# Performance work log

Hardware: AMD Instinct MI355X
Metric: run time of the kernel (lower is better)

The kernel has to match this reference:

```python
import jax, jax.numpy as jnp
import numpy as np

B, NC, CN, K, DN = 2, 256, 256, 16, 64
G, HM, HS, HMOD, MOD_OUT = 8, 128, 128, 64, 5


def setup_inputs() -> dict:
    rng = np.random.default_rng(0)
    # per-neuron top-K neighbors within cell, excluding self, sorted (matches torch buffer build)
    scores = rng.random((NC, CN, CN)).astype(np.float32)
    ii = np.arange(CN)
    scores[:, ii, ii] = -np.inf
    conn = np.argpartition(-scores, K, axis=-1)[..., :K]
    conn = np.sort(conn, axis=-1).astype(np.int32)  # [NC, CN, K]

    key = jax.random.key(0)
    ks = jax.random.split(key, 12)
    n = lambda k, s, sc=1.0: jax.random.normal(k, s, jnp.float32) * sc
    return {
        'h': n(ks[0], (B, NC, CN, DN), 0.01),
        'w_conn': n(ks[1], (B, NC, CN, K), 0.1),
        'cell_context': n(ks[2], (B, NC, DN), 0.1),
        'neuron_id': n(ks[3], (NC, CN, DN), 0.02),
        'msg_w1': n(ks[4], (G, HM, 3 * DN), 0.05), 'msg_b1': jnp.zeros((G, HM)),
        'msg_w2': n(ks[5], (G, DN, HM), 0.005), 'msg_b2': jnp.zeros((G, DN)),
        'state_w1': n(ks[6], (G, HS, 3 * DN), 0.05), 'state_b1': jnp.zeros((G, HS)),
        'state_w2': n(ks[7], (G, DN, HS), 0.005), 'state_b2': jnp.zeros((G, DN)),
        'mod_w1': n(ks[8], (NC, 2 * DN, HMOD), 0.05), 'mod_b1': jnp.zeros((NC, HMOD)),
        'mod_w2': n(ks[9], (NC, HMOD, MOD_OUT), 0.0005), 'mod_b2': jnp.zeros((NC, MOD_OUT)),
        'conn_idx': jnp.asarray(conn),
        'cell_to_group': (jnp.arange(NC) % G).astype(jnp.int32),
    }


def reference(h, w_conn, cell_context, neuron_id,
              msg_w1, msg_b1, msg_w2, msg_b2,
              state_w1, state_b1, state_w2, state_b2,
              mod_w1, mod_b1, mod_w2, mod_b2,
              conn_idx, cell_to_group):
    nc = h.shape[1]
    cell_ix = jnp.arange(nc)[:, None, None]
    # gather K-neighbor states per neuron: [B, NC, CN, K, DN]
    nb = jax.vmap(lambda hb: hb[cell_ix, conn_idx])(h)
    # connection-weighted aggregation
    agg = jnp.einsum('bnck,bnckd->bncd', w_conn, nb)

    g = cell_to_group  # [NC]
    # grouped message MLP (2-layer), per-cell weights gathered from group table
    mfeat = jnp.concatenate([h, agg, jnp.broadcast_to(neuron_id[None], h.shape)], axis=-1)
    mh = jax.nn.gelu(jnp.einsum('bncf,nhf->bnch', mfeat, msg_w1[g]) + msg_b1[g][None, :, None, :])
    msg = jnp.einsum('bnch,ndh->bncd', mh, msg_w2[g]) + msg_b2[g][None, :, None, :]

    # grouped state MLP, residual update on h
    ctx = jnp.broadcast_to(cell_context[:, :, None, :], h.shape)
    sfeat = jnp.concatenate([h, msg, ctx], axis=-1)
    sh = jax.nn.gelu(jnp.einsum('bncf,nhf->bnch', sfeat, state_w1[g]) + state_b1[g][None, :, None, :])
    h_new = h + jnp.einsum('bnch,ndh->bncd', sh, state_w2[g]) + state_b2[g][None, :, None, :]

    # per-cell modulation MLP on pooled stats (h_mean || msg_mean)
    pooled = jnp.concatenate([h_new.mean(axis=2), msg.mean(axis=2)], axis=-1)  # [B, NC, 2DN]
    ph = jax.nn.gelu(jnp.einsum('bnf,nfh->bnh', pooled, mod_w1) + mod_b1[None])
    mod = jnp.einsum('bnh,nho->bno', ph, mod_w2) + mod_b2[None]
    return h_new, msg, mod
```

## Files before the change

### kernel.cpp

```cpp
#include <hip/hip_runtime.h>

#define NC_  256
#define CN_  256
#define K_   16
#define DN_  64
#define G_   8
#define HM_  128
#define F3_  192

typedef unsigned short u16;
typedef short v8s __attribute__((ext_vector_type(8)));
typedef float v4f __attribute__((ext_vector_type(4)));


__device__ __forceinline__ u16 f2b(float f) {
    unsigned v; __builtin_memcpy(&v, &f, 4);
    v = v + 0x7fffu + ((v >> 16) & 1u);
    return (u16)(v >> 16);
}
__device__ __forceinline__ v8s cvt8(const float* p) {
    float4 a = *(const float4*)p, b = *(const float4*)(p + 4);
    v8s r;
    r[0] = (short)f2b(a.x); r[1] = (short)f2b(a.y); r[2] = (short)f2b(a.z); r[3] = (short)f2b(a.w);
    r[4] = (short)f2b(b.x); r[5] = (short)f2b(b.y); r[6] = (short)f2b(b.z); r[7] = (short)f2b(b.w);
    return r;
}
__device__ __forceinline__ float gelu_t(float x) {
    float u = x * x;
    float t = 1.5957691216057308f * x * __builtin_fmaf(0.044715f, u, 1.0f);
    float e = __expf(-t);
    return x * __builtin_amdgcn_rcpf(1.0f + e);
}

__global__ __launch_bounds__(256) void cvt_w(
    const float* __restrict__ mw1, const float* __restrict__ mw2,
    const float* __restrict__ sw1, const float* __restrict__ sw2,
    u16* __restrict__ dst)
{
    int e = (blockIdx.x * 256 + threadIdx.x) * 4;
    const float* s; int off;
    if      (e < 196608) { s = mw1; off = e; }
    else if (e < 262144) { s = mw2; off = e - 196608; }
    else if (e < 458752) { s = sw1; off = e - 262144; }
    else                 { s = sw2; off = e - 458752; }
    float4 v = *(const float4*)(s + off);
    ushort4 o4;
    o4.x = f2b(v.x); o4.y = f2b(v.y); o4.z = f2b(v.z); o4.w = f2b(v.w);
    *(ushort4*)(dst + e) = o4;
}

__global__ __launch_bounds__(256) void gth(
    const float* __restrict__ h, const float* __restrict__ wconn,
    const int* __restrict__ conn, float* __restrict__ outf)
{
    __shared__ u16 hl[16384];
    const int p    = blockIdx.x;
    const int bnc  = (p & 7) * 64 + ((p >> 3) & 63);
    const int half = p >> 9;
    const int tid  = threadIdx.x;
    const int wave = tid >> 6, lane = tid & 63;
    const int r0   = half * 128 + wave * 32;
    const int n    = bnc & 255;
    const size_t hb = (size_t)bnc * 16384;

#pragma unroll
    for (int i = 0; i < 16; ++i) {
        float4 v = *(const float4*)(h + hb + tid * 4 + i * 1024);
        ushort4 o;
        o.x = f2b(v.x); o.y = f2b(v.y); o.z = f2b(v.z); o.w = f2b(v.w);
        *(ushort4*)(hl + tid * 4 + i * 1024) = o;
    }
    __syncthreads();

    float* aggo = outf + (size_t)8388608 + hb;
    const int*   __restrict__ cp = conn  + n * 4096 + r0 * 16;
    const float* __restrict__ wp = wconn + (size_t)bnc * 4096 + (size_t)r0 * 16;
    int iv = cp[lane]; float wv = wp[lane];
    for (int g4 = 0; g4 < 8; ++g4) {
        int ivn = 0; float wvn = 0.0f;
        if (g4 < 7) { ivn = cp[(g4 + 1) * 64 + lane]; wvn = wp[(g4 + 1) * 64 + lane]; }
#pragma unroll
        for (int r = 0; r < 4; ++r) {
            float a0 = 0.0f, a1 = 0.0f;
#pragma unroll
            for (int k = 0; k < 16; k += 2) {
                const int l0 = r * 16 + k;
                int   i0 = __builtin_amdgcn_readlane(iv, l0);
                int   i1 = __builtin_amdgcn_readlane(iv, l0 + 1);
                float w0 = __int_as_float(__builtin_amdgcn_readlane(__float_as_int(wv), l0));
                float w1 = __int_as_float(__builtin_amdgcn_readlane(__float_as_int(wv), l0 + 1));
                unsigned h0 = (unsigned)hl[i0 * 64 + lane] << 16;
                unsigned h1 = (unsigned)hl[i1 * 64 + lane] << 16;
                a0 = __builtin_fmaf(w0, __uint_as_float(h0), a0);
                a1 = __builtin_fmaf(w1, __uint_as_float(h1), a1);
            }
            aggo[(size_t)(r0 + g4 * 4 + r) * 64 + lane] = a0 + a1;
        }
        iv = ivn; wv = wvn;
    }
}

__global__ __launch_bounds__(64, 4) void mg_main(
    const float* __restrict__ h,    const float* __restrict__ ctx,
    const float* __restrict__ nid,
    const u16* __restrict__ mw1b,   const float* __restrict__ mb1,
    const u16* __restrict__ mw2b,   const float* __restrict__ mb2,
    const u16* __restrict__ sw1b,   const float* __restrict__ sb1,
    const u16* __restrict__ sw2b,   const float* __restrict__ sb2,
    const int* __restrict__ c2g,
    float* __restrict__ outf,       float* __restrict__ partial)
{
    const int p     = blockIdx.x;
    const int bnc   = (p & 7) * 64 + (p >> 6);
    const int chunk = (p >> 3) & 7;
    const int r0    = chunk * 32;
    const int n     = bnc & 255;
    const int g     = c2g[n];
    const int lane  = threadIdx.x;
    const int q     = lane >> 4, ln = lane & 15;

    __shared__ u16 buf[32 * 138];

    const size_t hbase = (size_t)bnc * 16384;
    const size_t nbase = (size_t)n   * 16384;
    float* oH = outf + hbase;
    float* oM = outf + (size_t)8388608 + hbase;
    const size_t pbase = (size_t)(bnc * 8 + chunk) * 128;

    v8s hfr[2][2], gfr[2][2], nfr[2][2];
#pragma unroll
    for (int mi = 0; mi < 2; ++mi) {
        int c = r0 + mi * 16 + ln;
        hfr[mi][0] = cvt8(h   + hbase + (size_t)c * 64 +  0 + q * 8);
        hfr[mi][1] = cvt8(h   + hbase + (size_t)c * 64 + 32 + q * 8);
        gfr[mi][0] = cvt8(oM  + (size_t)c * 64 +  0 + q * 8);
        gfr[mi][1] = cvt8(oM  + (size_t)c * 64 + 32 + q * 8);
        nfr[mi][0] = cvt8(nid + nbase + (size_t)c * 64 +  0 + q * 8);
        nfr[mi][1] = cvt8(nid + nbase + (size_t)c * 64 + 32 + q * 8);
    }

    {
        v8s afr0[6] = {hfr[0][0], hfr[0][1], gfr[0][0], gfr[0][1], nfr[0][0], nfr[0][1]};
        v8s afr1[6] = {hfr[1][0], hfr[1][1], gfr[1][0], gfr[1][1], nfr[1][0], nfr[1][1]};
        float b1v[8];
#pragma unroll
        for (int nt = 0; nt < 8; ++nt) b1v[nt] = mb1[g * HM_ + nt * 16 + ln];
        const u16* w1g = mw1b + (size_t)g * HM_ * F3_;
#pragma unroll
        for (int nt = 0; nt < 8; ++nt) {
            v4f acc0 = {0,0,0,0}, acc1 = {0,0,0,0};
#pragma unroll
            for (int ks = 0; ks < 6; ++ks) {
                v8s bf = *(const v8s*)(w1g + (nt * 16 + ln) * F3_ + ks * 32 + q * 8);
                acc0 = __builtin_amdgcn_mfma_f32_16x16x32_bf16(afr0[ks], bf, acc0, 0, 0, 0);
                acc1 = __builtin_amdgcn_mfma_f32_16x16x32_bf16(afr1[ks], bf, acc1, 0, 0, 0);
            }
            int c0 = q * 4, c1 = 16 + q * 4;
#pragma unroll
            for (int r = 0; r < 4; ++r) {
                buf[(c0 + r) * 138 + nt * 16 + ln] = f2b(gelu_t(acc0[r] + b1v[nt]));
                buf[(c1 + r) * 138 + nt * 16 + ln] = f2b(gelu_t(acc1[r] + b1v[nt]));
            }
        }
    }

    {
        v8s afr[2][4];
#pragma unroll
        for (int mi = 0; mi < 2; ++mi) {
            int c = mi * 16 + ln;
#pragma unroll
            for (int ks = 0; ks < 4; ++ks)
                afr[mi][ks] = *(const v8s*)(buf + c * 138 + ks * 32 + q * 8);
        }
        const u16* w2g = mw2b + (size_t)g * DN_ * HM_;
        float mpart[4];
#pragma unroll
        for (int nt = 0; nt < 4; ++nt) {
            float bb = mb2[g * DN_ + nt * 16 + ln];
            v4f acc[2] = {{0,0,0,0},{0,0,0,0}};
#pragma unroll
            for (int ks = 0; ks < 4; ++ks) {
                v8s bf = *(const v8s*)(w2g + (nt * 16 + ln) * HM_ + ks * 32 + q * 8);
#pragma unroll
                for (int mi = 0; mi < 2; ++mi)
                    acc[mi] = __builtin_amdgcn_mfma_f32_16x16x32_bf16(afr[mi][ks], bf, acc[mi], 0, 0, 0);
            }
            float ms = 0.0f;
            int d = nt * 16 + ln;
#pragma unroll
            for (int mi = 0; mi < 2; ++mi) {
                int c = mi * 16 + q * 4;
#pragma unroll
                for (int r = 0; r < 4; ++r) {
                    float mv = acc[mi][r] + bb;
                    buf[(c + r) * 138 + d] = f2b(mv);
                    oM[(size_t)(r0 + c + r) * 64 + d] = mv;
                    ms += mv;
                }
            }
            mpart[nt] = ms;
        }
#pragma unroll
        for (int nt = 0; nt < 4; ++nt) {
            float v = mpart[nt];
            v += __shfl_xor(v, 16);
            v += __shfl_xor(v, 32);
            if (q == 0) partial[pbase + 64 + nt * 16 + ln] = v * (1.0f / 256.0f);
        }
    }

    {
        v8s cfr0 = cvt8(ctx + (size_t)bnc * DN_ +  0 + q * 8);
        v8s cfr1 = cvt8(ctx + (size_t)bnc * DN_ + 32 + q * 8);
        v8s afr[2][4];
#pragma unroll
        for (int mi = 0; mi < 2; ++mi) {
            int c = mi * 16 + ln;
            afr[mi][0] = hfr[mi][0];
            afr[mi][1] = hfr[mi][1];
            afr[mi][2] = *(const v8s*)(buf + c * 138 +  0 + q * 8);
            afr[mi][3] = *(const v8s*)(buf + c * 138 + 32 + q * 8);
        }
        float b1v[8];
#pragma unroll
        for (int nt = 0; nt < 8; ++nt) b1v[nt] = sb1[g * HM_ + nt * 16 + ln];
        const u16* w1g = sw1b + (size_t)g * HM_ * F3_;
#pragma unroll
        for (int nt = 0; nt < 8; ++nt) {
            v4f acc[2] = {{0,0,0,0},{0,0,0,0}};
#pragma unroll
            for (int ks = 0; ks < 4; ++ks) {
                v8s bf = *(const v8s*)(w1g + (nt * 16 + ln) * F3_ + ks * 32 + q * 8);
#pragma unroll
                for (int mi = 0; mi < 2; ++mi)
                    acc[mi] = __builtin_amdgcn_mfma_f32_16x16x32_bf16(afr[mi][ks], bf, acc[mi], 0, 0, 0);
            }
#pragma unroll
            for (int ks = 4; ks < 6; ++ks) {
                v8s bf = *(const v8s*)(w1g + (nt * 16 + ln) * F3_ + ks * 32 + q * 8);
                v8s aa = (ks == 4) ? cfr0 : cfr1;
#pragma unroll
                for (int mi = 0; mi < 2; ++mi)
                    acc[mi] = __builtin_amdgcn_mfma_f32_16x16x32_bf16(aa, bf, acc[mi], 0, 0, 0);
            }
#pragma unroll
            for (int mi = 0; mi < 2; ++mi) {
                int c = mi * 16 + q * 4;
#pragma unroll
                for (int r = 0; r < 4; ++r)
                    buf[(c + r) * 138 + nt * 16 + ln] = f2b(gelu_t(acc[mi][r] + b1v[nt]));
            }
        }
    }

    {
        v8s afr[2][4];
#pragma unroll
        for (int mi = 0; mi < 2; ++mi) {
            int c = mi * 16 + ln;
#pragma unroll
            for (int ks = 0; ks < 4; ++ks)
                afr[mi][ks] = *(const v8s*)(buf + c * 138 + ks * 32 + q * 8);
        }
        const u16* w2g = sw2b + (size_t)g * DN_ * HM_;
        float hpart[4];
#pragma unroll
        for (int nt = 0; nt < 4; ++nt) {
            float bb = sb2[g * DN_ + nt * 16 + ln];
            v4f acc[2] = {{0,0,0,0},{0,0,0,0}};
#pragma unroll
            for (int ks = 0; ks < 4; ++ks) {
                v8s bf = *(const v8s*)(w2g + (nt * 16 + ln) * HM_ + ks * 32 + q * 8);
#pragma unroll
                for (int mi = 0; mi < 2; ++mi)
                    acc[mi] = __builtin_amdgcn_mfma_f32_16x16x32_bf16(afr[mi][ks], bf, acc[mi], 0, 0, 0);
            }
            float hs = 0.0f;
            int d = nt * 16 + ln;
#pragma unroll
            for (int mi = 0; mi < 2; ++mi) {
                int c = mi * 16 + q * 4;
#pragma unroll
                for (int r = 0; r < 4; ++r) {
                    float hv = h[hbase + (size_t)(r0 + c + r) * 64 + d];
                    float hn = hv + acc[mi][r] + bb;
                    oH[(size_t)(r0 + c + r) * 64 + d] = hn;
                    hs += hn;
                }
            }
            hpart[nt] = hs;
        }
#pragma unroll
        for (int nt = 0; nt < 4; ++nt) {
            float v = hpart[nt];
            v += __shfl_xor(v, 16);
            v += __shfl_xor(v, 32);
            if (q == 0) partial[pbase + nt * 16 + ln] = v * (1.0f / 256.0f);
        }
    }
}

__global__ __launch_bounds__(256) void mg_mod(
    const float* __restrict__ w1, const float* __restrict__ b1,
    const float* __restrict__ w2, const float* __restrict__ b2,
    const float* __restrict__ partial, float* __restrict__ outf)
{
    __shared__ float pool[128];
    __shared__ float ph4[4][64];
    const int bnc = blockIdx.x, n = bnc & 255, t = threadIdx.x;
    if (t < 128) {
        const float* pp = partial + (size_t)bnc * 1024 + t;
        float s = 0.0f;
#pragma unroll
        for (int j = 0; j < 8; ++j) s += pp[j * 128];
        pool[t] = s;
    }
    __syncthreads();
    {
        const int col = t & 63, fh = t >> 6;
        const float* w1p = w1 + ((size_t)n * 128 + fh * 32) * 64 + col;
        float acc = 0.0f;
#pragma unroll
        for (int i = 0; i < 32; ++i)
            acc = __builtin_fmaf(pool[fh * 32 + i], w1p[(size_t)i * 64], acc);
        ph4[fh][col] = acc;
    }
    __syncthreads();
    if (t < 64) {
        float a  = ph4[0][t] + ph4[1][t] + ph4[2][t] + ph4[3][t] + b1[n * 64 + t];
        float ph = gelu_t(a);
        float part5[5];
#pragma unroll
        for (int o = 0; o < 5; ++o) part5[o] = ph * w2[((size_t)n * 64 + t) * 5 + o];
#pragma unroll
        for (int off = 32; off > 0; off >>= 1)
#pragma unroll
            for (int o = 0; o < 5; ++o) part5[o] += __shfl_down(part5[o], off);
        if (t == 0) {
#pragma unroll
            for (int o = 0; o < 5; ++o)
                outf[(size_t)16777216 + bnc * 5 + o] = part5[o] + b2[n * 5 + o];
        }
    }
}

extern "C" void kernel_launch(void* const* d_in, const int* in_sizes, int n_in,
                              void* d_out, int out_size, void* d_ws, size_t ws_size,
                              hipStream_t stream) {
    const float* h     = (const float*)d_in[0];
    const float* wconn = (const float*)d_in[1];
    const float* ctx   = (const float*)d_in[2];
    const float* nid   = (const float*)d_in[3];
    const float* mw1   = (const float*)d_in[4];
    const float* mb1   = (const float*)d_in[5];
    const float* mw2   = (const float*)d_in[6];
    const float* mb2   = (const float*)d_in[7];
    const float* sw1   = (const float*)d_in[8];
    const float* sb1   = (const float*)d_in[9];
    const float* sw2   = (const float*)d_in[10];
    const float* sb2   = (const float*)d_in[11];
    const float* dw1   = (const float*)d_in[12];
    const float* db1   = (const float*)d_in[13];
    const float* dw2   = (const float*)d_in[14];
    const float* db2   = (const float*)d_in[15];
    const int* conn    = (const int*)d_in[16];
    const int* c2g     = (const int*)d_in[17];
    float* outf    = (float*)d_out;
    u16*   wb      = (u16*)d_ws;
    float* partial = (float*)((char*)d_ws + 1048576);

    cvt_w<<<512, 256, 0, stream>>>(mw1, mw2, sw1, sw2, wb);
    gth<<<1024, 256, 0, stream>>>(h, wconn, conn, outf);
    mg_main<<<4096, 64, 0, stream>>>(h, ctx, nid,
                                     wb,           mb1,
                                     wb + 196608,  mb2,
                                     wb + 262144,  sb1,
                                     wb + 458752,  sb2,
                                     c2g, outf, partial);
    mg_mod<<<512, 256, 0, stream>>>(dw1, db1, dw2, db2, partial, outf);
}
```

Measured before the change: 243.2 us.

## Fuse neighbor gather into main MLP kernel with 64-row tiles per block

Removes the separate gather kernel. The weighted neighbor aggregation is now computed inside mg_main directly from global h, and written as bf16 into shared memory instead of round-tripping fp32 agg through the output buffer. Each 64-thread block now handles 64 rows instead of 32, with 4 MFMA row tiles, which halves the grid and the partial-sum count used by the modulation kernel. The trade-offs are per-lane scattered global loads for the gather instead of LDS reads, more registers per wave (launch bounds lowered to 2), and fewer blocks available to hide latency.

```diff
diff --git a/kernel.cpp b/kernel.cpp
--- a/kernel.cpp
+++ b/kernel.cpp
@@ -49,125 +49,104 @@
     *(ushort4*)(dst + e) = o4;
 }
 
-__global__ __launch_bounds__(256) void gth(
-    const float* __restrict__ h, const float* __restrict__ wconn,
-    const int* __restrict__ conn, float* __restrict__ outf)
-{
-    __shared__ u16 hl[16384];
-    const int p    = blockIdx.x;
-    const int bnc  = (p & 7) * 64 + ((p >> 3) & 63);
-    const int half = p >> 9;
-    const int tid  = threadIdx.x;
-    const int wave = tid >> 6, lane = tid & 63;
-    const int r0   = half * 128 + wave * 32;
-    const int n    = bnc & 255;
-    const size_t hb = (size_t)bnc * 16384;
-
-#pragma unroll
-    for (int i = 0; i < 16; ++i) {
-        float4 v = *(const float4*)(h + hb + tid * 4 + i * 1024);
-        ushort4 o;
-        o.x = f2b(v.x); o.y = f2b(v.y); o.z = f2b(v.z); o.w = f2b(v.w);
-        *(ushort4*)(hl + tid * 4 + i * 1024) = o;
-    }
-    __syncthreads();
-
-    float* aggo = outf + (size_t)8388608 + hb;
-    const int*   __restrict__ cp = conn  + n * 4096 + r0 * 16;
-    const float* __restrict__ wp = wconn + (size_t)bnc * 4096 + (size_t)r0 * 16;
-    int iv = cp[lane]; float wv = wp[lane];
-    for (int g4 = 0; g4 < 8; ++g4) {
-        int ivn = 0; float wvn = 0.0f;
-        if (g4 < 7) { ivn = cp[(g4 + 1) * 64 + lane]; wvn = wp[(g4 + 1) * 64 + lane]; }
-#pragma unroll
-        for (int r = 0; r < 4; ++r) {
-            float a0 = 0.0f, a1 = 0.0f;
-#pragma unroll
-            for (int k = 0; k < 16; k += 2) {
-                const int l0 = r * 16 + k;
-                int   i0 = __builtin_amdgcn_readlane(iv, l0);
-                int   i1 = __builtin_amdgcn_readlane(iv, l0 + 1);
-                float w0 = __int_as_float(__builtin_amdgcn_readlane(__float_as_int(wv), l0));
-                float w1 = __int_as_float(__builtin_amdgcn_readlane(__float_as_int(wv), l0 + 1));
-                unsigned h0 = (unsigned)hl[i0 * 64 + lane] << 16;
-                unsigned h1 = (unsigned)hl[i1 * 64 + lane] << 16;
-                a0 = __builtin_fmaf(w0, __uint_as_float(h0), a0);
-                a1 = __builtin_fmaf(w1, __uint_as_float(h1), a1);
-            }
-            aggo[(size_t)(r0 + g4 * 4 + r) * 64 + lane] = a0 + a1;
-        }
-        iv = ivn; wv = wvn;
-    }
-}
-
-__global__ __launch_bounds__(64, 4) void mg_main(
-    const float* __restrict__ h,    const float* __restrict__ ctx,
-    const float* __restrict__ nid,
+__global__ __launch_bounds__(64, 2) void mg_main(
+    const float* __restrict__ h,    const float* __restrict__ wconn,
+    const float* __restrict__ ctx,  const float* __restrict__ nid,
     const u16* __restrict__ mw1b,   const float* __restrict__ mb1,
     const u16* __restrict__ mw2b,   const float* __restrict__ mb2,
     const u16* __restrict__ sw1b,   const float* __restrict__ sb1,
     const u16* __restrict__ sw2b,   const float* __restrict__ sb2,
-    const int* __restrict__ c2g,
+    const int* __restrict__ conn,   const int* __restrict__ c2g,
     float* __restrict__ outf,       float* __restrict__ partial)
 {
     const int p     = blockIdx.x;
-    const int bnc   = (p & 7) * 64 + (p >> 6);
-    const int chunk = (p >> 3) & 7;
-    const int r0    = chunk * 32;
+    const int bnc   = (p & 7) * 64 + (p >> 5);
+    const int quart = (p >> 3) & 3;
+    const int r0    = quart * 64;
     const int n     = bnc & 255;
     const int g     = c2g[n];
     const int lane  = threadIdx.x;
     const int q     = lane >> 4, ln = lane & 15;
 
-    __shared__ u16 buf[32 * 138];
+    __shared__ u16 buf[64 * 138];
 
     const size_t hbase = (size_t)bnc * 16384;
     const size_t nbase = (size_t)n   * 16384;
     float* oH = outf + hbase;
     float* oM = outf + (size_t)8388608 + hbase;
-    const size_t pbase = (size_t)(bnc * 8 + chunk) * 128;
-
-    v8s hfr[2][2], gfr[2][2], nfr[2][2];
-#pragma unroll
-    for (int mi = 0; mi < 2; ++mi) {
-        int c = r0 + mi * 16 + ln;
-        hfr[mi][0] = cvt8(h   + hbase + (size_t)c * 64 +  0 + q * 8);
-        hfr[mi][1] = cvt8(h   + hbase + (size_t)c * 64 + 32 + q * 8);
-        gfr[mi][0] = cvt8(oM  + (size_t)c * 64 +  0 + q * 8);
-        gfr[mi][1] = cvt8(oM  + (size_t)c * 64 + 32 + q * 8);
+    const size_t pbase = (size_t)(bnc * 4 + quart) * 128;
+
+    {
+        const float* __restrict__ hp = h + hbase;
+        const int*   __restrict__ cp = conn  + n * 4096 + r0 * 16;
+        const float* __restrict__ wp = wconn + (size_t)bnc * 4096 + (size_t)r0 * 16;
+        int iv = cp[lane]; float wv = wp[lane];
+        for (int g4 = 0; g4 < 16; ++g4) {
+            int ivn = 0; float wvn = 0.0f;
+            if (g4 < 15) { ivn = cp[(g4 + 1) * 64 + lane]; wvn = wp[(g4 + 1) * 64 + lane]; }
+#pragma unroll
+            for (int r = 0; r < 4; ++r) {
+                float a0 = 0.0f, a1 = 0.0f;
+#pragma unroll
+                for (int k = 0; k < 16; k += 2) {
+                    const int l0 = r * 16 + k;
+                    int   i0 = __builtin_amdgcn_readlane(iv, l0);
+                    int   i1 = __builtin_amdgcn_readlane(iv, l0 + 1);
+                    float w0 = __int_as_float(__builtin_amdgcn_readlane(__float_as_int(wv), l0));
+                    float w1 = __int_as_float(__builtin_amdgcn_readlane(__float_as_int(wv), l0 + 1));
+                    a0 = __builtin_fmaf(w0, hp[i0 * 64 + lane], a0);
+                    a1 = __builtin_fmaf(w1, hp[i1 * 64 + lane], a1);
+                }
+                buf[(g4 * 4 + r) * 138 + lane] = f2b(a0 + a1);
+            }
+            iv = ivn; wv = wvn;
+        }
+    }
+
+    v8s hfr[4][2], gfr[4][2], nfr[4][2];
+#pragma unroll
+    for (int mi = 0; mi < 4; ++mi) {
+        int c  = r0 + mi * 16 + ln;
+        int lc = mi * 16 + ln;
+        hfr[mi][0] = cvt8(h + hbase + (size_t)c * 64 +  0 + q * 8);
+        hfr[mi][1] = cvt8(h + hbase + (size_t)c * 64 + 32 + q * 8);
+        gfr[mi][0] = *(const v8s*)(buf + lc * 138 +  0 + q * 8);
+        gfr[mi][1] = *(const v8s*)(buf + lc * 138 + 32 + q * 8);
         nfr[mi][0] = cvt8(nid + nbase + (size_t)c * 64 +  0 + q * 8);
         nfr[mi][1] = cvt8(nid + nbase + (size_t)c * 64 + 32 + q * 8);
     }
 
     {
-        v8s afr0[6] = {hfr[0][0], hfr[0][1], gfr[0][0], gfr[0][1], nfr[0][0], nfr[0][1]};
-        v8s afr1[6] = {hfr[1][0], hfr[1][1], gfr[1][0], gfr[1][1], nfr[1][0], nfr[1][1]};
         float b1v[8];
 #pragma unroll
         for (int nt = 0; nt < 8; ++nt) b1v[nt] = mb1[g * HM_ + nt * 16 + ln];
         const u16* w1g = mw1b + (size_t)g * HM_ * F3_;
 #pragma unroll
         for (int nt = 0; nt < 8; ++nt) {
-            v4f acc0 = {0,0,0,0}, acc1 = {0,0,0,0};
+            v4f acc[4] = {{0,0,0,0},{0,0,0,0},{0,0,0,0},{0,0,0,0}};
 #pragma unroll
             for (int ks = 0; ks < 6; ++ks) {
                 v8s bf = *(const v8s*)(w1g + (nt * 16 + ln) * F3_ + ks * 32 + q * 8);
-                acc0 = __builtin_amdgcn_mfma_f32_16x16x32_bf16(afr0[ks], bf, acc0, 0, 0, 0);
-                acc1 = __builtin_amdgcn_mfma_f32_16x16x32_bf16(afr1[ks], bf, acc1, 0, 0, 0);
-            }
-            int c0 = q * 4, c1 = 16 + q * 4;
-#pragma unroll
-            for (int r = 0; r < 4; ++r) {
-                buf[(c0 + r) * 138 + nt * 16 + ln] = f2b(gelu_t(acc0[r] + b1v[nt]));
-                buf[(c1 + r) * 138 + nt * 16 + ln] = f2b(gelu_t(acc1[r] + b1v[nt]));
-            }
-        }
-    }
-
-    {
-        v8s afr[2][4];
-#pragma unroll
-        for (int mi = 0; mi < 2; ++mi) {
+#pragma unroll
+                for (int mi = 0; mi < 4; ++mi) {
+                    v8s aa = (ks < 2) ? hfr[mi][ks] : (ks < 4) ? gfr[mi][ks - 2] : nfr[mi][ks - 4];
+                    acc[mi] = __builtin_amdgcn_mfma_f32_16x16x32_bf16(aa, bf, acc[mi], 0, 0, 0);
+                }
+            }
+#pragma unroll
+            for (int mi = 0; mi < 4; ++mi) {
+                int c = mi * 16 + q * 4;
+#pragma unroll
+                for (int r = 0; r < 4; ++r)
+                    buf[(c + r) * 138 + nt * 16 + ln] = f2b(gelu_t(acc[mi][r] + b1v[nt]));
+            }
+        }
+    }
+
+    {
+        v8s afr[4][4];
+#pragma unroll
+        for (int mi = 0; mi < 4; ++mi) {
             int c = mi * 16 + ln;
 #pragma unroll
             for (int ks = 0; ks < 4; ++ks)
@@ -178,18 +157,18 @@
 #pragma unroll
         for (int nt = 0; nt < 4; ++nt) {
             float bb = mb2[g * DN_ + nt * 16 + ln];
-            v4f acc[2] = {{0,0,0,0},{0,0,0,0}};
+            v4f acc[4] = {{0,0,0,0},{0,0,0,0},{0,0,0,0},{0,0,0,0}};
 #pragma unroll
             for (int ks = 0; ks < 4; ++ks) {
                 v8s bf = *(const v8s*)(w2g + (nt * 16 + ln) * HM_ + ks * 32 + q * 8);
 #pragma unroll
-                for (int mi = 0; mi < 2; ++mi)
+                for (int mi = 0; mi < 4; ++mi)
                     acc[mi] = __builtin_amdgcn_mfma_f32_16x16x32_bf16(afr[mi][ks], bf, acc[mi], 0, 0, 0);
             }
             float ms = 0.0f;
             int d = nt * 16 + ln;
 #pragma unroll
-            for (int mi = 0; mi < 2; ++mi) {
+            for (int mi = 0; mi < 4; ++mi) {
                 int c = mi * 16 + q * 4;
 #pragma unroll
                 for (int r = 0; r < 4; ++r) {
@@ -213,14 +192,12 @@
     {
         v8s cfr0 = cvt8(ctx + (size_t)bnc * DN_ +  0 + q * 8);
         v8s cfr1 = cvt8(ctx + (size_t)bnc * DN_ + 32 + q * 8);
-        v8s afr[2][4];
-#pragma unroll
-        for (int mi = 0; mi < 2; ++mi) {
+        v8s mfr[4][2];
+#pragma unroll
+        for (int mi = 0; mi < 4; ++mi) {
             int c = mi * 16 + ln;
-            afr[mi][0] = hfr[mi][0];
-            afr[mi][1] = hfr[mi][1];
-            afr[mi][2] = *(const v8s*)(buf + c * 138 +  0 + q * 8);
-            afr[mi][3] = *(const v8s*)(buf + c * 138 + 32 + q * 8);
+            mfr[mi][0] = *(const v8s*)(buf + c * 138 +  0 + q * 8);
+            mfr[mi][1] = *(const v8s*)(buf + c * 138 + 32 + q * 8);
         }
         float b1v[8];
 #pragma unroll
@@ -228,24 +205,26 @@
         const u16* w1g = sw1b + (size_t)g * HM_ * F3_;
 #pragma unroll
         for (int nt = 0; nt < 8; ++nt) {
-            v4f acc[2] = {{0,0,0,0},{0,0,0,0}};
+            v4f acc[4] = {{0,0,0,0},{0,0,0,0},{0,0,0,0},{0,0,0,0}};
 #pragma unroll
             for (int ks = 0; ks < 4; ++ks) {
                 v8s bf = *(const v8s*)(w1g + (nt * 16 + ln) * F3_ + ks * 32 + q * 8);
 #pragma unroll
-                for (int mi = 0; mi < 2; ++mi)
-                    acc[mi] = __builtin_amdgcn_mfma_f32_16x16x32_bf16(afr[mi][ks], bf, acc[mi], 0, 0, 0);
+                for (int mi = 0; mi < 4; ++mi) {
+                    v8s aa = (ks < 2) ? hfr[mi][ks] : mfr[mi][ks - 2];
+                    acc[mi] = __builtin_amdgcn_mfma_f32_16x16x32_bf16(aa, bf, acc[mi], 0, 0, 0);
+                }
             }
 #pragma unroll
             for (int ks = 4; ks < 6; ++ks) {
                 v8s bf = *(const v8s*)(w1g + (nt * 16 + ln) * F3_ + ks * 32 + q * 8);
                 v8s aa = (ks == 4) ? cfr0 : cfr1;
 #pragma unroll
-                for (int mi = 0; mi < 2; ++mi)
+                for (int mi = 0; mi < 4; ++mi)
                     acc[mi] = __builtin_amdgcn_mfma_f32_16x16x32_bf16(aa, bf, acc[mi], 0, 0, 0);
             }
 #pragma unroll
-            for (int mi = 0; mi < 2; ++mi) {
+            for (int mi = 0; mi < 4; ++mi) {
                 int c = mi * 16 + q * 4;
 #pragma unroll
                 for (int r = 0; r < 4; ++r)
@@ -255,9 +234,9 @@
     }
 
     {
-        v8s afr[2][4];
-#pragma unroll
-        for (int mi = 0; mi < 2; ++mi) {
+        v8s afr[4][4];
+#pragma unroll
+        for (int mi = 0; mi < 4; ++mi) {
             int c = mi * 16 + ln;
 #pragma unroll
             for (int ks = 0; ks < 4; ++ks)
@@ -268,18 +247,18 @@
 #pragma unroll
         for (int nt = 0; nt < 4; ++nt) {
             float bb = sb2[g * DN_ + nt * 16 + ln];
-            v4f acc[2] = {{0,0,0,0},{0,0,0,0}};
+            v4f acc[4] = {{0,0,0,0},{0,0,0,0},{0,0,0,0},{0,0,0,0}};
 #pragma unroll
             for (int ks = 0; ks < 4; ++ks) {
                 v8s bf = *(const v8s*)(w2g + (nt * 16 + ln) * HM_ + ks * 32 + q * 8);
 #pragma unroll
-                for (int mi = 0; mi < 2; ++mi)
+                for (int mi = 0; mi < 4; ++mi)
                     acc[mi] = __builtin_amdgcn_mfma_f32_16x16x32_bf16(afr[mi][ks], bf, acc[mi], 0, 0, 0);
             }
             float hs = 0.0f;
             int d = nt * 16 + ln;
 #pragma unroll
-            for (int mi = 0; mi < 2; ++mi) {
+            for (int mi = 0; mi < 4; ++mi) {
                 int c = mi * 16 + q * 4;
 #pragma unroll
                 for (int r = 0; r < 4; ++r) {
@@ -310,10 +289,10 @@
     __shared__ float ph4[4][64];
     const int bnc = blockIdx.x, n = bnc & 255, t = threadIdx.x;
     if (t < 128) {
-        const float* pp = partial + (size_t)bnc * 1024 + t;
+        const float* pp = partial + (size_t)bnc * 512 + t;
         float s = 0.0f;
 #pragma unroll
-        for (int j = 0; j < 8; ++j) s += pp[j * 128];
+        for (int j = 0; j < 4; ++j) s += pp[j * 128];
         pool[t] = s;
     }
     __syncthreads();
@@ -371,12 +350,11 @@
     float* partial = (float*)((char*)d_ws + 1048576);
 
     cvt_w<<<512, 256, 0, stream>>>(mw1, mw2, sw1, sw2, wb);
-    gth<<<1024, 256, 0, stream>>>(h, wconn, conn, outf);
-    mg_main<<<4096, 64, 0, stream>>>(h, ctx, nid,
+    mg_main<<<2048, 64, 0, stream>>>(h, wconn, ctx, nid,
                                      wb,           mb1,
                                      wb + 196608,  mb2,
                                      wb + 262144,  sb1,
                                      wb + 458752,  sb2,
-                                     c2g, outf, partial);
+                                     conn, c2g, outf, partial);
     mg_mod<<<512, 256, 0, stream>>>(dw1, db1, dw2, db2, partial, outf);
 }
```

New measurement: 216.2 us, median of 2. -11.1%, faster.

## Fuse neighbor gather-aggregation into main MLP kernel, dropping separate gather launch

Applied to the files above, without the earlier changes.

Removes the standalone gather kernel, which staged the whole cell's h in LDS as bf16 and wrote agg to the msg output buffer. Each mg_main block now computes agg for its 32 neurons directly from global h (fp32), using scalar-broadcast conn and weight loads, and keeps the result in the LDS buffer as bf16. The MLP then reads it as an MFMA fragment. This saves a kernel launch and the agg write/readback round trip. In exchange, each 64-thread block issues many dependent global gathers per neuron with little parallelism, which may raise latency. Neighbor h rows also get re-read from L2 by the 8 chunks that share a cell.

```diff
diff --git a/kernel.cpp b/kernel.cpp
--- a/kernel.cpp
+++ b/kernel.cpp
@@ -49,65 +49,14 @@
     *(ushort4*)(dst + e) = o4;
 }
 
-__global__ __launch_bounds__(256) void gth(
-    const float* __restrict__ h, const float* __restrict__ wconn,
-    const int* __restrict__ conn, float* __restrict__ outf)
-{
-    __shared__ u16 hl[16384];
-    const int p    = blockIdx.x;
-    const int bnc  = (p & 7) * 64 + ((p >> 3) & 63);
-    const int half = p >> 9;
-    const int tid  = threadIdx.x;
-    const int wave = tid >> 6, lane = tid & 63;
-    const int r0   = half * 128 + wave * 32;
-    const int n    = bnc & 255;
-    const size_t hb = (size_t)bnc * 16384;
-
-#pragma unroll
-    for (int i = 0; i < 16; ++i) {
-        float4 v = *(const float4*)(h + hb + tid * 4 + i * 1024);
-        ushort4 o;
-        o.x = f2b(v.x); o.y = f2b(v.y); o.z = f2b(v.z); o.w = f2b(v.w);
-        *(ushort4*)(hl + tid * 4 + i * 1024) = o;
-    }
-    __syncthreads();
-
-    float* aggo = outf + (size_t)8388608 + hb;
-    const int*   __restrict__ cp = conn  + n * 4096 + r0 * 16;
-    const float* __restrict__ wp = wconn + (size_t)bnc * 4096 + (size_t)r0 * 16;
-    int iv = cp[lane]; float wv = wp[lane];
-    for (int g4 = 0; g4 < 8; ++g4) {
-        int ivn = 0; float wvn = 0.0f;
-        if (g4 < 7) { ivn = cp[(g4 + 1) * 64 + lane]; wvn = wp[(g4 + 1) * 64 + lane]; }
-#pragma unroll
-        for (int r = 0; r < 4; ++r) {
-            float a0 = 0.0f, a1 = 0.0f;
-#pragma unroll
-            for (int k = 0; k < 16; k += 2) {
-                const int l0 = r * 16 + k;
-                int   i0 = __builtin_amdgcn_readlane(iv, l0);
-                int   i1 = __builtin_amdgcn_readlane(iv, l0 + 1);
-                float w0 = __int_as_float(__builtin_amdgcn_readlane(__float_as_int(wv), l0));
-                float w1 = __int_as_float(__builtin_amdgcn_readlane(__float_as_int(wv), l0 + 1));
-                unsigned h0 = (unsigned)hl[i0 * 64 + lane] << 16;
-                unsigned h1 = (unsigned)hl[i1 * 64 + lane] << 16;
-                a0 = __builtin_fmaf(w0, __uint_as_float(h0), a0);
-                a1 = __builtin_fmaf(w1, __uint_as_float(h1), a1);
-            }
-            aggo[(size_t)(r0 + g4 * 4 + r) * 64 + lane] = a0 + a1;
-        }
-        iv = ivn; wv = wvn;
-    }
-}
-
 __global__ __launch_bounds__(64, 4) void mg_main(
-    const float* __restrict__ h,    const float* __restrict__ ctx,
-    const float* __restrict__ nid,
+    const float* __restrict__ h,    const float* __restrict__ wconn,
+    const float* __restrict__ ctx,  const float* __restrict__ nid,
     const u16* __restrict__ mw1b,   const float* __restrict__ mb1,
     const u16* __restrict__ mw2b,   const float* __restrict__ mb2,
     const u16* __restrict__ sw1b,   const float* __restrict__ sb1,
     const u16* __restrict__ sw2b,   const float* __restrict__ sb2,
-    const int* __restrict__ c2g,
+    const int* __restrict__ conn,   const int* __restrict__ c2g,
     float* __restrict__ outf,       float* __restrict__ partial)
 {
     const int p     = blockIdx.x;
@@ -127,14 +76,34 @@
     float* oM = outf + (size_t)8388608 + hbase;
     const size_t pbase = (size_t)(bnc * 8 + chunk) * 128;
 
+    {
+        const float* __restrict__ hp = h + hbase;
+        const int*   __restrict__ cp = conn  + n * 4096 + r0 * 16;
+        const float* __restrict__ wp = wconn + (size_t)bnc * 4096 + (size_t)r0 * 16;
+        for (int c = 0; c < 32; ++c) {
+            float acc0 = 0.0f, acc1 = 0.0f;
+#pragma unroll
+            for (int k = 0; k < 16; k += 2) {
+                int   i0 = cp[c * 16 + k];
+                int   i1 = cp[c * 16 + k + 1];
+                float w0 = wp[c * 16 + k];
+                float w1 = wp[c * 16 + k + 1];
+                acc0 = __builtin_fmaf(w0, hp[i0 * 64 + lane], acc0);
+                acc1 = __builtin_fmaf(w1, hp[i1 * 64 + lane], acc1);
+            }
+            buf[c * 138 + lane] = f2b(acc0 + acc1);
+        }
+    }
+
     v8s hfr[2][2], gfr[2][2], nfr[2][2];
 #pragma unroll
     for (int mi = 0; mi < 2; ++mi) {
-        int c = r0 + mi * 16 + ln;
-        hfr[mi][0] = cvt8(h   + hbase + (size_t)c * 64 +  0 + q * 8);
-        hfr[mi][1] = cvt8(h   + hbase + (size_t)c * 64 + 32 + q * 8);
-        gfr[mi][0] = cvt8(oM  + (size_t)c * 64 +  0 + q * 8);
-        gfr[mi][1] = cvt8(oM  + (size_t)c * 64 + 32 + q * 8);
+        int c  = r0 + mi * 16 + ln;
+        int lc = mi * 16 + ln;
+        hfr[mi][0] = cvt8(h + hbase + (size_t)c * 64 +  0 + q * 8);
+        hfr[mi][1] = cvt8(h + hbase + (size_t)c * 64 + 32 + q * 8);
+        gfr[mi][0] = *(const v8s*)(buf + lc * 138 +  0 + q * 8);
+        gfr[mi][1] = *(const v8s*)(buf + lc * 138 + 32 + q * 8);
         nfr[mi][0] = cvt8(nid + nbase + (size_t)c * 64 +  0 + q * 8);
         nfr[mi][1] = cvt8(nid + nbase + (size_t)c * 64 + 32 + q * 8);
     }
@@ -213,14 +182,12 @@
     {
         v8s cfr0 = cvt8(ctx + (size_t)bnc * DN_ +  0 + q * 8);
         v8s cfr1 = cvt8(ctx + (size_t)bnc * DN_ + 32 + q * 8);
-        v8s afr[2][4];
+        v8s mfr[2][2];
 #pragma unroll
         for (int mi = 0; mi < 2; ++mi) {
             int c = mi * 16 + ln;
-            afr[mi][0] = hfr[mi][0];
-            afr[mi][1] = hfr[mi][1];
-            afr[mi][2] = *(const v8s*)(buf + c * 138 +  0 + q * 8);
-            afr[mi][3] = *(const v8s*)(buf + c * 138 + 32 + q * 8);
+            mfr[mi][0] = *(const v8s*)(buf + c * 138 +  0 + q * 8);
+            mfr[mi][1] = *(const v8s*)(buf + c * 138 + 32 + q * 8);
         }
         float b1v[8];
 #pragma unroll
@@ -233,8 +200,10 @@
             for (int ks = 0; ks < 4; ++ks) {
                 v8s bf = *(const v8s*)(w1g + (nt * 16 + ln) * F3_ + ks * 32 + q * 8);
 #pragma unroll
-                for (int mi = 0; mi < 2; ++mi)
-                    acc[mi] = __builtin_amdgcn_mfma_f32_16x16x32_bf16(afr[mi][ks], bf, acc[mi], 0, 0, 0);
+                for (int mi = 0; mi < 2; ++mi) {
+                    v8s aa = (ks < 2) ? hfr[mi][ks] : mfr[mi][ks - 2];
+                    acc[mi] = __builtin_amdgcn_mfma_f32_16x16x32_bf16(aa, bf, acc[mi], 0, 0, 0);
+                }
             }
 #pragma unroll
             for (int ks = 4; ks < 6; ++ks) {
@@ -371,12 +340,11 @@
     float* partial = (float*)((char*)d_ws + 1048576);
 
     cvt_w<<<512, 256, 0, stream>>>(mw1, mw2, sw1, sw2, wb);
-    gth<<<1024, 256, 0, stream>>>(h, wconn, conn, outf);
-    mg_main<<<4096, 64, 0, stream>>>(h, ctx, nid,
+    mg_main<<<4096, 64, 0, stream>>>(h, wconn, ctx, nid,
                                      wb,           mb1,
                                      wb + 196608,  mb2,
                                      wb + 262144,  sb1,
                                      wb + 458752,  sb2,
-                                     c2g, outf, partial);
+                                     conn, c2g, outf, partial);
     mg_mod<<<512, 256, 0, stream>>>(dw1, db1, dw2, db2, partial, outf);
 }
```

New measurement: 264.9 us. +8.9%, slower.
